# Kernel optimization log

Measured on AMD Instinct MI355X. Metric: run time of the kernel, lower is better.

The kernel has to match this reference:

```python
import jax, jax.numpy as jnp
import numpy as np

N_NODES = 50000
DEGREE = 32
NUM_FEATS = 128
NUM_HIDDEN = 128
NUM_LABELS = 40


def setup_inputs() -> dict:
    key = jax.random.key(0)
    k1, k2, k3, k4, k5, k6 = jax.random.split(key, 6)
    feats = jax.random.normal(k1, (N_NODES, NUM_FEATS), dtype=jnp.float32)
    neigh = jax.random.randint(k2, (N_NODES, DEGREE), 0, N_NODES, dtype=jnp.int32)
    batch = jnp.arange(N_NODES, dtype=jnp.int32)
    s1 = 1.0 / np.sqrt(2 * NUM_FEATS)
    s2 = 1.0 / np.sqrt(2 * NUM_HIDDEN)
    W1 = jax.random.uniform(k3, (2 * NUM_FEATS, NUM_HIDDEN), jnp.float32, -s1, s1)
    b1 = jax.random.uniform(k4, (NUM_HIDDEN,), jnp.float32, -s1, s1)
    W2 = jax.random.uniform(k5, (2 * NUM_HIDDEN, NUM_LABELS), jnp.float32, -s2, s2)
    b2 = jax.random.uniform(k6, (NUM_LABELS,), jnp.float32, -s2, s2)
    return {"feats": feats, "neigh": neigh, "batch": batch,
            "W1": W1, "b1": b1, "W2": W2, "b2": b2}


def reference(feats, neigh, batch, W1, b1, W2, b2):
    # Layer 1 (GraphConvolution with mean aggregator, relu; dropout in eval mode = identity).
    # Compute gc1 embeddings for ALL nodes once: identical math to the per-node
    # Python loop since the mean aggregator is deterministic.
    nbr_mean1 = jnp.take(feats, neigh, axis=0).mean(axis=1)          # [N, F]
    z1 = jnp.concatenate([feats, nbr_mean1], axis=-1)                # [N, 2F]
    h1 = jax.nn.relu(z1 @ W1 + b1)                                   # [N, H]
    # Layer 2 (no activation): concat self embedding with mean of neighbor embeddings.
    nbr_mean2 = jnp.take(h1, neigh[batch], axis=0).mean(axis=1)      # [B, H]
    z2 = jnp.concatenate([h1[batch], nbr_mean2], axis=-1)            # [B, 2H]
    return z2 @ W2 + b2                                              # [B, L]
```

## Files before the change

### kernel.cpp

```cpp
#include <hip/hip_runtime.h>
#include <hip/hip_bf16.h>

typedef __attribute__((ext_vector_type(8))) short short8;
typedef __attribute__((ext_vector_type(4))) float f32x4;

#define NFEAT 128
#define DEG 32
#define FSCALE 24.0f
#define FDEC (1.0f / (24.0f * 32.0f))
#define YSCALE 64.0f
#define YDEC (1.0f / (64.0f * 32.0f))

static __device__ __forceinline__ unsigned short f2bf(float f) {
    unsigned u = __float_as_uint(f);
    u += 0x7fffu + ((u >> 16) & 1u);
    return (unsigned short)(u >> 16);
}
static __device__ __forceinline__ int sxt8(unsigned x) {
    return (int)(signed char)(x & 0xffu);
}

__global__ void prep_feats_kernel(const float* __restrict__ in,
                                  unsigned short* __restrict__ outb,
                                  unsigned* __restrict__ out8, int n4) {
    int i = blockIdx.x * blockDim.x + threadIdx.x;
    if (i >= n4) return;
    float4 f = ((const float4*)in)[i];
    ushort4 ob;
    ob.x = f2bf(f.x); ob.y = f2bf(f.y); ob.z = f2bf(f.z); ob.w = f2bf(f.w);
    ((ushort4*)outb)[i] = ob;
    int a = max(-127, min(127, __float2int_rn(f.x * FSCALE)));
    int b = max(-127, min(127, __float2int_rn(f.y * FSCALE)));
    int c = max(-127, min(127, __float2int_rn(f.z * FSCALE)));
    int d = max(-127, min(127, __float2int_rn(f.w * FSCALE)));
    out8[i] = (unsigned)(a & 0xff) | ((unsigned)(b & 0xff) << 8) |
              ((unsigned)(c & 0xff) << 16) | ((unsigned)(d & 0xff) << 24);
}

__global__ void pack_w1_kernel(const float* __restrict__ W,
                               unsigned short* __restrict__ out) {
    int t = blockIdx.x * blockDim.x + threadIdx.x;
    if (t >= 8 * 8 * 64 * 8) return;
    int j    = t & 7;
    int lane = (t >> 3) & 63;
    int ks   = (t >> 9) & 7;
    int nt   = t >> 12;
    int k    = ks * 32 + (lane >> 4) * 8 + j;
    int col  = nt * 16 + (lane & 15);
    out[t] = f2bf(W[k * 128 + col]);
}

__global__ void pack_w2_kernel(const float* __restrict__ W2,
                               unsigned short* __restrict__ out, int L) {
    int t = blockIdx.x * blockDim.x + threadIdx.x;
    if (t >= 7 * 4 * 64 * 8) return;
    int j    = t & 7;
    int lane = (t >> 3) & 63;
    int ks   = (t >> 9) & 3;
    int nt   = t >> 11;
    int k    = ks * 32 + (lane >> 4) * 8 + j;
    int p    = nt * 16 + (lane & 15);
    float v = 0.f;
    if (p < 48) { if (p < L) v = W2[k * L + p]; }
    else        { int c = p - 48; if (c < L) v = W2[(128 + k) * L + c]; }
    out[t] = f2bf(v);
}

__global__ __launch_bounds__(256, 4) void gcn_layer1_kernel(
    const unsigned short* __restrict__ tableb,
    const unsigned char* __restrict__ table8,
    const int* __restrict__ neigh,
    const unsigned short* __restrict__ Wp,
    const float* __restrict__ bias,
    unsigned short* __restrict__ outp,
    int nRows)
{
    __shared__ unsigned int z1[16 * 128];
    const int tid = threadIdx.x;
    const int w = tid >> 6;
    const int l = tid & 63;
    const int g = l >> 4;
    const int c = l & 15;

    int srow = tid >> 4, sch = tid & 15;
    int sr = min(blockIdx.x * 16 + srow, nRows - 1);
    uint4 selfv = ((const uint4*)(tableb + (size_t)sr * NFEAT))[sch];

    const int r0 = blockIdx.x * 16 + w * 4;
    const int rc0 = min(r0 + 0, nRows - 1);
    const int rc1 = min(r0 + 1, nRows - 1);
    const int rc2 = min(r0 + 2, nRows - 1);
    const int rc3 = min(r0 + 3, nRows - 1);
    const int4* nb0 = (const int4*)(neigh + (size_t)rc0 * DEG);
    const int4* nb1 = (const int4*)(neigh + (size_t)rc1 * DEG);
    const int4* nb2 = (const int4*)(neigh + (size_t)rc2 * DEG);
    const int4* nb3 = (const int4*)(neigh + (size_t)rc3 * DEG);
    int4 ia0 = nb0[2 * g], ib0 = nb0[2 * g + 1];
    int4 ia1 = nb1[2 * g], ib1 = nb1[2 * g + 1];
    int4 ia2 = nb2[2 * g], ib2 = nb2[2 * g + 1];
    int4 ia3 = nb3[2 * g], ib3 = nb3[2 * g + 1];

    const char* tb8 = (const char*)table8;
    const size_t co8 = (size_t)(8 * c);
#define GLD(j) (*(const uint2*)(tb8 + (size_t)(j) * 128 + co8))
#define GATH(A, ia, ib) \
    uint2 A##0 = GLD(ia.x), A##1 = GLD(ia.y), A##2 = GLD(ia.z), A##3 = GLD(ia.w); \
    uint2 A##4 = GLD(ib.x), A##5 = GLD(ib.y), A##6 = GLD(ib.z), A##7 = GLD(ib.w);

    GATH(vA, ia0, ib0)
    GATH(vB, ia1, ib1)

    *(uint4*)((char*)z1 + srow * 512 + ((16 * sch) ^ ((srow & 7) << 4))) = selfv;

    int iacc[8];
#define CONSUME(A, rowi)                                                         \
    {                                                                            \
        _Pragma("unroll") for (int k = 0; k < 8; ++k) iacc[k] = 0;               \
        _Pragma("unroll") for (int q = 0; q < 8; ++q) {                          \
            uint2 v = (q==0)?A##0:(q==1)?A##1:(q==2)?A##2:(q==3)?A##3             \
                    :(q==4)?A##4:(q==5)?A##5:(q==6)?A##6:A##7;                   \
            unsigned x = v.x, y = v.y;                                           \
            iacc[0] += sxt8(x);       iacc[1] += sxt8(x >> 8);                   \
            iacc[2] += sxt8(x >> 16); iacc[3] += sxt8(x >> 24);                  \
            iacc[4] += sxt8(y);       iacc[5] += sxt8(y >> 8);                   \
            iacc[6] += sxt8(y >> 16); iacc[7] += sxt8(y >> 24);                  \
        }                                                                        \
        _Pragma("unroll") for (int k = 0; k < 8; ++k) iacc[k] += __shfl_xor(iacc[k], 16); \
        _Pragma("unroll") for (int k = 0; k < 8; ++k) iacc[k] += __shfl_xor(iacc[k], 32); \
        if (g == 0) {                                                            \
            int row = w * 4 + rowi;                                              \
            uint4 mb;                                                            \
            unsigned* mw = (unsigned*)&mb;                                       \
            _Pragma("unroll") for (int k = 0; k < 4; ++k) {                      \
                unsigned lo = f2bf((float)iacc[2 * k] * FDEC);                   \
                unsigned hi = f2bf((float)iacc[2 * k + 1] * FDEC);               \
                mw[k] = (hi << 16) | lo;                                         \
            }                                                                    \
            int byte = (256 + 16 * c) ^ ((row & 7) << 4);                        \
            *(uint4*)((char*)z1 + row * 512 + byte) = mb;                        \
        }                                                                        \
    }

    CONSUME(vA, 0)
    GATH(vC, ia2, ib2)
    CONSUME(vB, 1)
    GATH(vD, ia3, ib3)
    CONSUME(vC, 2)
    CONSUME(vD, 3)
#undef GLD
#undef GATH
#undef CONSUME
    __syncthreads();

    f32x4 macc0 = (f32x4){0.f,0.f,0.f,0.f}, macc1 = (f32x4){0.f,0.f,0.f,0.f};
    const int arow = l & 15;
    const int aswz = (arow & 7) << 4;
    const char* zbase = (const char*)z1 + arow * 512;

#pragma unroll
    for (int ks = 0; ks < 8; ++ks) {
        int kb = (ks * 64 + ((l >> 4) * 16)) ^ aswz;
        short8 a = *(const short8*)(zbase + kb);
        short8 b0 = *(const short8*)(Wp + ((size_t)((w * 2 + 0) * 8 + ks) * 64 + l) * 8);
        short8 b1 = *(const short8*)(Wp + ((size_t)((w * 2 + 1) * 8 + ks) * 64 + l) * 8);
        macc0 = __builtin_amdgcn_mfma_f32_16x16x32_bf16(a, b0, macc0, 0, 0, 0);
        macc1 = __builtin_amdgcn_mfma_f32_16x16x32_bf16(a, b1, macc1, 0, 0, 0);
    }

#pragma unroll
    for (int tt = 0; tt < 2; ++tt) {
        int col = (w * 2 + tt) * 16 + (l & 15);
        float bv = bias[col];
        f32x4 m = tt ? macc1 : macc0;
#pragma unroll
        for (int r2 = 0; r2 < 4; ++r2) {
            int row = blockIdx.x * 16 + (l >> 4) * 4 + r2;
            if (row < nRows) {
                float v = fmaxf(m[r2] + bv, 0.f);
                outp[(size_t)row * NFEAT + col] = f2bf(v);
            }
        }
    }
}

__global__ __launch_bounds__(256) void gemm2_kernel(
    const unsigned short* __restrict__ h1b,
    const unsigned short* __restrict__ W2p,
    const float* __restrict__ b2,
    float* __restrict__ X2,
    signed char* __restrict__ Y2,
    int nRows, int L)
{
    __shared__ unsigned int lds[64 * 64];
    const int tid = threadIdx.x, w = tid >> 6, l = tid & 63;

#pragma unroll
    for (int it = 0; it < 4; ++it) {
        int byte = tid * 16 + it * 4096;
        int row = byte >> 8, col = byte & 255;
        int r = min(blockIdx.x * 64 + row, nRows - 1);
        uint4 v = *(const uint4*)(h1b + (size_t)r * 128 + (col >> 1));
        *(uint4*)((char*)lds + row * 256 + (col ^ ((row & 7) << 4))) = v;
    }
    __syncthreads();

    f32x4 acc[7];
#pragma unroll
    for (int nt = 0; nt < 7; ++nt) acc[nt] = (f32x4){0.f,0.f,0.f,0.f};
    const int arow = w * 16 + (l & 15);
    const int aswz = (arow & 7) << 4;
    const char* zb = (const char*)lds + arow * 256;

#pragma unroll
    for (int ks = 0; ks < 4; ++ks) {
        short8 a = *(const short8*)(zb + ((ks * 64 + ((l >> 4) * 16)) ^ aswz));
#pragma unroll
        for (int nt = 0; nt < 7; ++nt) {
            short8 b = *(const short8*)(W2p + ((size_t)(nt * 4 + ks) * 64 + l) * 8);
            acc[nt] = __builtin_amdgcn_mfma_f32_16x16x32_bf16(a, b, acc[nt], 0, 0, 0);
        }
    }

#pragma unroll
    for (int nt = 0; nt < 7; ++nt) {
        int col = nt * 16 + (l & 15);
#pragma unroll
        for (int r2 = 0; r2 < 4; ++r2) {
            int row = blockIdx.x * 64 + w * 16 + (l >> 4) * 4 + r2;
            if (row >= nRows) continue;
            float v = acc[nt][r2];
            if (col < 48) {
                if (col < L) X2[(size_t)row * L + col] = v + b2[col];
            } else {
                int q = max(-127, min(127, __float2int_rn(v * YSCALE)));
                Y2[(size_t)row * 64 + (col - 48)] = (signed char)q;
            }
        }
    }
}

__global__ __launch_bounds__(256) void agg2_kernel(
    const float* __restrict__ X2,
    const unsigned char* __restrict__ Y2,
    const int* __restrict__ neigh,
    const int* __restrict__ batch,
    float* __restrict__ out,
    int nRows, int L)
{
    const int tid = threadIdx.x, w = tid >> 6, l = tid & 63;
    const int jg = l >> 3;
    const int c = l & 7;

    const int r0 = blockIdx.x * 16 + w * 4;
    int s[4];
    const int* nb[4];
#pragma unroll
    for (int rr = 0; rr < 4; ++rr) {
        int rc = min(r0 + rr, nRows - 1);
        s[rr] = batch[rc];
        nb[rr] = neigh + (size_t)s[rr] * DEG;
    }
    const char* yb = (const char*)Y2;
    const size_t co = (size_t)(8 * c);
#define YLD(j) (*(const uint2*)(yb + (size_t)(j) * 64 + co))

    uint2 v0[4], v1[4], v2[4], v3[4];
#pragma unroll
    for (int rr = 0; rr < 4; ++rr) {
        v0[rr] = YLD(nb[rr][jg]);
        v1[rr] = YLD(nb[rr][8 + jg]);
        v2[rr] = YLD(nb[rr][16 + jg]);
        v3[rr] = YLD(nb[rr][24 + jg]);
    }
#undef YLD

#pragma unroll
    for (int rr = 0; rr < 4; ++rr) {
        int iacc[8];
#pragma unroll
        for (int k = 0; k < 8; ++k) iacc[k] = 0;
#pragma unroll
        for (int q = 0; q < 4; ++q) {
            uint2 v = (q == 0) ? v0[rr] : (q == 1) ? v1[rr] : (q == 2) ? v2[rr] : v3[rr];
            unsigned x = v.x, y = v.y;
            iacc[0] += sxt8(x);       iacc[1] += sxt8(x >> 8);
            iacc[2] += sxt8(x >> 16); iacc[3] += sxt8(x >> 24);
            iacc[4] += sxt8(y);       iacc[5] += sxt8(y >> 8);
            iacc[6] += sxt8(y >> 16); iacc[7] += sxt8(y >> 24);
        }
#pragma unroll
        for (int k = 0; k < 8; ++k) {
            iacc[k] += __shfl_xor(iacc[k], 8);
            iacc[k] += __shfl_xor(iacc[k], 16);
            iacc[k] += __shfl_xor(iacc[k], 32);
        }
        int r = r0 + rr;
        if (jg == 0 && 8 * c < L && r < nRows) {
#pragma unroll
            for (int hv = 0; hv < 2; ++hv) {
                int colb = 8 * c + 4 * hv;
                if (colb < L) {
                    float4 xv = *(const float4*)(X2 + (size_t)s[rr] * L + colb);
                    float4 o;
                    o.x = xv.x + (float)iacc[4 * hv + 0] * YDEC;
                    o.y = xv.y + (float)iacc[4 * hv + 1] * YDEC;
                    o.z = xv.z + (float)iacc[4 * hv + 2] * YDEC;
                    o.w = xv.w + (float)iacc[4 * hv + 3] * YDEC;
                    *(float4*)(out + (size_t)r * L + colb) = o;
                }
            }
        }
    }
}

extern "C" void kernel_launch(void* const* d_in, const int* in_sizes, int n_in,
                              void* d_out, int out_size, void* d_ws, size_t ws_size,
                              hipStream_t stream) {
    const float* feats = (const float*)d_in[0];
    const int*   neigh = (const int*)d_in[1];
    const int*   batch = (const int*)d_in[2];
    const float* W1    = (const float*)d_in[3];
    const float* b1    = (const float*)d_in[4];
    const float* W2    = (const float*)d_in[5];
    const float* b2    = (const float*)d_in[6];

    const int N = in_sizes[0] / NFEAT;
    const int B = in_sizes[2];
    const int L = in_sizes[6];

    char* ws = (char*)d_ws;
    size_t off = 0;
    unsigned short* featsb = (unsigned short*)(ws + off); off += (size_t)N * NFEAT * 2;
    unsigned short* h1b    = (unsigned short*)(ws + off); off += (size_t)N * NFEAT * 2;
    float*          X2     = (float*)(ws + off);          off += (size_t)N * L * 4;
    signed char*    Y2     = (signed char*)(ws + off);    off += (size_t)N * 64;
    unsigned char*  feats8 = (unsigned char*)(ws + off);  off += (size_t)N * NFEAT;
    unsigned short* W1p    = (unsigned short*)(ws + off); off += 8 * 8 * 64 * 8 * 2;
    unsigned short* W2p    = (unsigned short*)(ws + off); off += 7 * 4 * 64 * 8 * 2;

    int n4 = N * NFEAT / 4;
    prep_feats_kernel<<<(n4 + 255) / 256, 256, 0, stream>>>(
        feats, featsb, (unsigned*)feats8, n4);
    pack_w1_kernel<<<(8 * 8 * 64 * 8 + 255) / 256, 256, 0, stream>>>(W1, W1p);
    pack_w2_kernel<<<(7 * 4 * 64 * 8 + 255) / 256, 256, 0, stream>>>(W2, W2p, L);

    gcn_layer1_kernel<<<(N + 15) / 16, 256, 0, stream>>>(
        featsb, feats8, neigh, W1p, b1, h1b, N);

    gemm2_kernel<<<(N + 63) / 64, 256, 0, stream>>>(
        h1b, W2p, b2, X2, Y2, N, L);

    agg2_kernel<<<(B + 15) / 16, 256, 0, stream>>>(
        X2, (const unsigned char*)Y2, neigh, batch, (float*)d_out, B, L);
}
```

Measured before the change: 149.6 us.

## Fuse layer-1 GEMM with layer-2 projection and merge prep kernels

Layer 1 and the second-layer GEMM now run in one kernel: the relu'd h1 tile is written back into shared memory and immediately multiplied by packed W2, so the bf16 h1 buffer is no longer written to or read from global memory. The three prep/pack kernels are merged into one launch, which saves launch overhead. The int8 neighbor gather now loads 16 bytes per lane from 8 neighbor groups instead of 8 bytes from 4. The cost is extra syncthreads and lower per-block GEMM2 efficiency: tiles are 16 rows instead of 64, and one wave computes a single W2 tile.

```diff
diff --git a/kernel.cpp b/kernel.cpp
--- a/kernel.cpp
+++ b/kernel.cpp
@@ -20,215 +20,209 @@
     return (int)(signed char)(x & 0xffu);
 }
 
-__global__ void prep_feats_kernel(const float* __restrict__ in,
-                                  unsigned short* __restrict__ outb,
-                                  unsigned* __restrict__ out8, int n4) {
-    int i = blockIdx.x * blockDim.x + threadIdx.x;
-    if (i >= n4) return;
-    float4 f = ((const float4*)in)[i];
-    ushort4 ob;
-    ob.x = f2bf(f.x); ob.y = f2bf(f.y); ob.z = f2bf(f.z); ob.w = f2bf(f.w);
-    ((ushort4*)outb)[i] = ob;
-    int a = max(-127, min(127, __float2int_rn(f.x * FSCALE)));
-    int b = max(-127, min(127, __float2int_rn(f.y * FSCALE)));
-    int c = max(-127, min(127, __float2int_rn(f.z * FSCALE)));
-    int d = max(-127, min(127, __float2int_rn(f.w * FSCALE)));
-    out8[i] = (unsigned)(a & 0xff) | ((unsigned)(b & 0xff) << 8) |
-              ((unsigned)(c & 0xff) << 16) | ((unsigned)(d & 0xff) << 24);
-}
-
-__global__ void pack_w1_kernel(const float* __restrict__ W,
-                               unsigned short* __restrict__ out) {
-    int t = blockIdx.x * blockDim.x + threadIdx.x;
-    if (t >= 8 * 8 * 64 * 8) return;
-    int j    = t & 7;
-    int lane = (t >> 3) & 63;
-    int ks   = (t >> 9) & 7;
-    int nt   = t >> 12;
-    int k    = ks * 32 + (lane >> 4) * 8 + j;
-    int col  = nt * 16 + (lane & 15);
-    out[t] = f2bf(W[k * 128 + col]);
-}
-
-__global__ void pack_w2_kernel(const float* __restrict__ W2,
-                               unsigned short* __restrict__ out, int L) {
-    int t = blockIdx.x * blockDim.x + threadIdx.x;
-    if (t >= 7 * 4 * 64 * 8) return;
-    int j    = t & 7;
-    int lane = (t >> 3) & 63;
-    int ks   = (t >> 9) & 3;
-    int nt   = t >> 11;
-    int k    = ks * 32 + (lane >> 4) * 8 + j;
-    int p    = nt * 16 + (lane & 15);
-    float v = 0.f;
-    if (p < 48) { if (p < L) v = W2[k * L + p]; }
-    else        { int c = p - 48; if (c < L) v = W2[(128 + k) * L + c]; }
-    out[t] = f2bf(v);
-}
-
-__global__ __launch_bounds__(256, 4) void gcn_layer1_kernel(
+__global__ void prep_all_kernel(const float* __restrict__ feats,
+                                unsigned short* __restrict__ featsb,
+                                unsigned* __restrict__ feats8,
+                                const float* __restrict__ W1,
+                                unsigned short* __restrict__ W1p,
+                                const float* __restrict__ W2,
+                                unsigned short* __restrict__ W2p,
+                                int n4, int nPrepBlocks, int L) {
+    int b = blockIdx.x;
+    if (b < nPrepBlocks) {
+        int i = b * 256 + threadIdx.x;
+        if (i < n4) {
+            float4 f = ((const float4*)feats)[i];
+            ushort4 ob;
+            ob.x = f2bf(f.x); ob.y = f2bf(f.y); ob.z = f2bf(f.z); ob.w = f2bf(f.w);
+            ((ushort4*)featsb)[i] = ob;
+            int a0 = max(-127, min(127, __float2int_rn(f.x * FSCALE)));
+            int a1 = max(-127, min(127, __float2int_rn(f.y * FSCALE)));
+            int a2 = max(-127, min(127, __float2int_rn(f.z * FSCALE)));
+            int a3 = max(-127, min(127, __float2int_rn(f.w * FSCALE)));
+            feats8[i] = (unsigned)(a0 & 0xff) | ((unsigned)(a1 & 0xff) << 8) |
+                        ((unsigned)(a2 & 0xff) << 16) | ((unsigned)(a3 & 0xff) << 24);
+        }
+    } else if (b < nPrepBlocks + 128) {
+        int t = (b - nPrepBlocks) * 256 + threadIdx.x;
+        int j    = t & 7;
+        int lane = (t >> 3) & 63;
+        int ks   = (t >> 9) & 7;
+        int nt   = t >> 12;
+        int k    = ks * 32 + (lane >> 4) * 8 + j;
+        int col  = nt * 16 + (lane & 15);
+        W1p[t] = f2bf(W1[k * 128 + col]);
+    } else {
+        int t = (b - nPrepBlocks - 128) * 256 + threadIdx.x;
+        if (t < 7 * 4 * 64 * 8) {
+            int j    = t & 7;
+            int lane = (t >> 3) & 63;
+            int ks   = (t >> 9) & 3;
+            int nt   = t >> 11;
+            int k    = ks * 32 + (lane >> 4) * 8 + j;
+            int p    = nt * 16 + (lane & 15);
+            float v = 0.f;
+            if (p < 48) { if (p < L) v = W2[k * L + p]; }
+            else        { int cc = p - 48; if (cc < L) v = W2[(128 + k) * L + cc]; }
+            W2p[t] = f2bf(v);
+        }
+    }
+}
+
+__global__ __launch_bounds__(256, 4) void layer1_fused_kernel(
     const unsigned short* __restrict__ tableb,
     const unsigned char* __restrict__ table8,
     const int* __restrict__ neigh,
-    const unsigned short* __restrict__ Wp,
-    const float* __restrict__ bias,
-    unsigned short* __restrict__ outp,
-    int nRows)
-{
-    __shared__ unsigned int z1[16 * 128];
-    const int tid = threadIdx.x;
-    const int w = tid >> 6;
-    const int l = tid & 63;
-    const int g = l >> 4;
-    const int c = l & 15;
-
-    int srow = tid >> 4, sch = tid & 15;
-    int sr = min(blockIdx.x * 16 + srow, nRows - 1);
-    uint4 selfv = ((const uint4*)(tableb + (size_t)sr * NFEAT))[sch];
-
-    const int r0 = blockIdx.x * 16 + w * 4;
-    const int rc0 = min(r0 + 0, nRows - 1);
-    const int rc1 = min(r0 + 1, nRows - 1);
-    const int rc2 = min(r0 + 2, nRows - 1);
-    const int rc3 = min(r0 + 3, nRows - 1);
-    const int4* nb0 = (const int4*)(neigh + (size_t)rc0 * DEG);
-    const int4* nb1 = (const int4*)(neigh + (size_t)rc1 * DEG);
-    const int4* nb2 = (const int4*)(neigh + (size_t)rc2 * DEG);
-    const int4* nb3 = (const int4*)(neigh + (size_t)rc3 * DEG);
-    int4 ia0 = nb0[2 * g], ib0 = nb0[2 * g + 1];
-    int4 ia1 = nb1[2 * g], ib1 = nb1[2 * g + 1];
-    int4 ia2 = nb2[2 * g], ib2 = nb2[2 * g + 1];
-    int4 ia3 = nb3[2 * g], ib3 = nb3[2 * g + 1];
-
-    const char* tb8 = (const char*)table8;
-    const size_t co8 = (size_t)(8 * c);
-#define GLD(j) (*(const uint2*)(tb8 + (size_t)(j) * 128 + co8))
-#define GATH(A, ia, ib) \
-    uint2 A##0 = GLD(ia.x), A##1 = GLD(ia.y), A##2 = GLD(ia.z), A##3 = GLD(ia.w); \
-    uint2 A##4 = GLD(ib.x), A##5 = GLD(ib.y), A##6 = GLD(ib.z), A##7 = GLD(ib.w);
-
-    GATH(vA, ia0, ib0)
-    GATH(vB, ia1, ib1)
-
-    *(uint4*)((char*)z1 + srow * 512 + ((16 * sch) ^ ((srow & 7) << 4))) = selfv;
-
-    int iacc[8];
-#define CONSUME(A, rowi)                                                         \
-    {                                                                            \
-        _Pragma("unroll") for (int k = 0; k < 8; ++k) iacc[k] = 0;               \
-        _Pragma("unroll") for (int q = 0; q < 8; ++q) {                          \
-            uint2 v = (q==0)?A##0:(q==1)?A##1:(q==2)?A##2:(q==3)?A##3             \
-                    :(q==4)?A##4:(q==5)?A##5:(q==6)?A##6:A##7;                   \
-            unsigned x = v.x, y = v.y;                                           \
-            iacc[0] += sxt8(x);       iacc[1] += sxt8(x >> 8);                   \
-            iacc[2] += sxt8(x >> 16); iacc[3] += sxt8(x >> 24);                  \
-            iacc[4] += sxt8(y);       iacc[5] += sxt8(y >> 8);                   \
-            iacc[6] += sxt8(y >> 16); iacc[7] += sxt8(y >> 24);                  \
-        }                                                                        \
-        _Pragma("unroll") for (int k = 0; k < 8; ++k) iacc[k] += __shfl_xor(iacc[k], 16); \
-        _Pragma("unroll") for (int k = 0; k < 8; ++k) iacc[k] += __shfl_xor(iacc[k], 32); \
-        if (g == 0) {                                                            \
-            int row = w * 4 + rowi;                                              \
-            uint4 mb;                                                            \
-            unsigned* mw = (unsigned*)&mb;                                       \
-            _Pragma("unroll") for (int k = 0; k < 4; ++k) {                      \
-                unsigned lo = f2bf((float)iacc[2 * k] * FDEC);                   \
-                unsigned hi = f2bf((float)iacc[2 * k + 1] * FDEC);               \
-                mw[k] = (hi << 16) | lo;                                         \
-            }                                                                    \
-            int byte = (256 + 16 * c) ^ ((row & 7) << 4);                        \
-            *(uint4*)((char*)z1 + row * 512 + byte) = mb;                        \
-        }                                                                        \
-    }
-
-    CONSUME(vA, 0)
-    GATH(vC, ia2, ib2)
-    CONSUME(vB, 1)
-    GATH(vD, ia3, ib3)
-    CONSUME(vC, 2)
-    CONSUME(vD, 3)
-#undef GLD
-#undef GATH
-#undef CONSUME
-    __syncthreads();
-
-    f32x4 macc0 = (f32x4){0.f,0.f,0.f,0.f}, macc1 = (f32x4){0.f,0.f,0.f,0.f};
-    const int arow = l & 15;
-    const int aswz = (arow & 7) << 4;
-    const char* zbase = (const char*)z1 + arow * 512;
-
-#pragma unroll
-    for (int ks = 0; ks < 8; ++ks) {
-        int kb = (ks * 64 + ((l >> 4) * 16)) ^ aswz;
-        short8 a = *(const short8*)(zbase + kb);
-        short8 b0 = *(const short8*)(Wp + ((size_t)((w * 2 + 0) * 8 + ks) * 64 + l) * 8);
-        short8 b1 = *(const short8*)(Wp + ((size_t)((w * 2 + 1) * 8 + ks) * 64 + l) * 8);
-        macc0 = __builtin_amdgcn_mfma_f32_16x16x32_bf16(a, b0, macc0, 0, 0, 0);
-        macc1 = __builtin_amdgcn_mfma_f32_16x16x32_bf16(a, b1, macc1, 0, 0, 0);
-    }
-
-#pragma unroll
-    for (int tt = 0; tt < 2; ++tt) {
-        int col = (w * 2 + tt) * 16 + (l & 15);
-        float bv = bias[col];
-        f32x4 m = tt ? macc1 : macc0;
-#pragma unroll
-        for (int r2 = 0; r2 < 4; ++r2) {
-            int row = blockIdx.x * 16 + (l >> 4) * 4 + r2;
-            if (row < nRows) {
-                float v = fmaxf(m[r2] + bv, 0.f);
-                outp[(size_t)row * NFEAT + col] = f2bf(v);
-            }
-        }
-    }
-}
-
-__global__ __launch_bounds__(256) void gemm2_kernel(
-    const unsigned short* __restrict__ h1b,
+    const unsigned short* __restrict__ W1p,
+    const float* __restrict__ b1,
     const unsigned short* __restrict__ W2p,
     const float* __restrict__ b2,
     float* __restrict__ X2,
     signed char* __restrict__ Y2,
     int nRows, int L)
 {
-    __shared__ unsigned int lds[64 * 64];
-    const int tid = threadIdx.x, w = tid >> 6, l = tid & 63;
-
-#pragma unroll
-    for (int it = 0; it < 4; ++it) {
-        int byte = tid * 16 + it * 4096;
-        int row = byte >> 8, col = byte & 255;
-        int r = min(blockIdx.x * 64 + row, nRows - 1);
-        uint4 v = *(const uint4*)(h1b + (size_t)r * 128 + (col >> 1));
-        *(uint4*)((char*)lds + row * 256 + (col ^ ((row & 7) << 4))) = v;
-    }
+    __shared__ unsigned int z1[16 * 128];
+    const int tid = threadIdx.x;
+    const int w = tid >> 6;
+    const int l = tid & 63;
+    const int jg = l >> 3;
+    const int c = l & 7;
+
+    int srow = tid >> 4, sch = tid & 15;
+    int sr = min(blockIdx.x * 16 + srow, nRows - 1);
+    uint4 selfv = ((const uint4*)(tableb + (size_t)sr * NFEAT))[sch];
+
+    const int r0 = blockIdx.x * 16 + w * 4;
+    const int* nbp0 = neigh + (size_t)min(r0 + 0, nRows - 1) * DEG;
+    const int* nbp1 = neigh + (size_t)min(r0 + 1, nRows - 1) * DEG;
+    const int* nbp2 = neigh + (size_t)min(r0 + 2, nRows - 1) * DEG;
+    const int* nbp3 = neigh + (size_t)min(r0 + 3, nRows - 1) * DEG;
+    int i00 = nbp0[jg], i01 = nbp0[8 + jg], i02 = nbp0[16 + jg], i03 = nbp0[24 + jg];
+    int i10 = nbp1[jg], i11 = nbp1[8 + jg], i12 = nbp1[16 + jg], i13 = nbp1[24 + jg];
+    int i20 = nbp2[jg], i21 = nbp2[8 + jg], i22 = nbp2[16 + jg], i23 = nbp2[24 + jg];
+    int i30 = nbp3[jg], i31 = nbp3[8 + jg], i32 = nbp3[16 + jg], i33 = nbp3[24 + jg];
+
+    const char* tb8 = (const char*)table8;
+    const size_t co = (size_t)(16 * c);
+#define GLD16(j) (*(const uint4*)(tb8 + (size_t)(j) * 128 + co))
+#define GATH4(A, a, b_, c_, d_) \
+    uint4 A##0 = GLD16(a), A##1 = GLD16(b_), A##2 = GLD16(c_), A##3 = GLD16(d_);
+
+    GATH4(vA, i00, i01, i02, i03)
+    GATH4(vB, i10, i11, i12, i13)
+
+    *(uint4*)((char*)z1 + srow * 512 + ((16 * sch) ^ ((srow & 7) << 4))) = selfv;
+
+    GATH4(vC, i20, i21, i22, i23)
+
+    int iacc[16];
+#define UNPK(v)                                                        \
+    {                                                                  \
+        iacc[0]  += sxt8(v.x);       iacc[1]  += sxt8(v.x >> 8);       \
+        iacc[2]  += sxt8(v.x >> 16); iacc[3]  += sxt8(v.x >> 24);      \
+        iacc[4]  += sxt8(v.y);       iacc[5]  += sxt8(v.y >> 8);       \
+        iacc[6]  += sxt8(v.y >> 16); iacc[7]  += sxt8(v.y >> 24);      \
+        iacc[8]  += sxt8(v.z);       iacc[9]  += sxt8(v.z >> 8);       \
+        iacc[10] += sxt8(v.z >> 16); iacc[11] += sxt8(v.z >> 24);      \
+        iacc[12] += sxt8(v.w);       iacc[13] += sxt8(v.w >> 8);       \
+        iacc[14] += sxt8(v.w >> 16); iacc[15] += sxt8(v.w >> 24);      \
+    }
+#define CONSUME16(A, rowi)                                                        \
+    {                                                                             \
+        _Pragma("unroll") for (int k = 0; k < 16; ++k) iacc[k] = 0;               \
+        UNPK(A##0) UNPK(A##1) UNPK(A##2) UNPK(A##3)                               \
+        _Pragma("unroll") for (int k = 0; k < 16; ++k) iacc[k] += __shfl_xor(iacc[k], 8);  \
+        _Pragma("unroll") for (int k = 0; k < 16; ++k) iacc[k] += __shfl_xor(iacc[k], 16); \
+        _Pragma("unroll") for (int k = 0; k < 16; ++k) iacc[k] += __shfl_xor(iacc[k], 32); \
+        if (jg == 0) {                                                            \
+            int row = w * 4 + rowi;                                               \
+            int swz = (row & 7) << 4;                                             \
+            uint4 m0, m1;                                                         \
+            unsigned* mw0 = (unsigned*)&m0;                                       \
+            unsigned* mw1 = (unsigned*)&m1;                                       \
+            _Pragma("unroll") for (int k = 0; k < 4; ++k) {                       \
+                mw0[k] = ((unsigned)f2bf((float)iacc[2 * k + 1] * FDEC) << 16) |  \
+                         (unsigned)f2bf((float)iacc[2 * k] * FDEC);               \
+                mw1[k] = ((unsigned)f2bf((float)iacc[2 * k + 9] * FDEC) << 16) |  \
+                         (unsigned)f2bf((float)iacc[2 * k + 8] * FDEC);           \
+            }                                                                     \
+            *(uint4*)((char*)z1 + row * 512 + ((256 + 32 * c) ^ swz)) = m0;       \
+            *(uint4*)((char*)z1 + row * 512 + ((256 + 32 * c + 16) ^ swz)) = m1;  \
+        }                                                                         \
+    }
+
+    CONSUME16(vA, 0)
+    GATH4(vD, i30, i31, i32, i33)
+    CONSUME16(vB, 1)
+    CONSUME16(vC, 2)
+    CONSUME16(vD, 3)
+#undef GLD16
+#undef GATH4
+#undef UNPK
+#undef CONSUME16
     __syncthreads();
 
-    f32x4 acc[7];
-#pragma unroll
-    for (int nt = 0; nt < 7; ++nt) acc[nt] = (f32x4){0.f,0.f,0.f,0.f};
-    const int arow = w * 16 + (l & 15);
-    const int aswz = (arow & 7) << 4;
-    const char* zb = (const char*)lds + arow * 256;
-
-#pragma unroll
-    for (int ks = 0; ks < 4; ++ks) {
-        short8 a = *(const short8*)(zb + ((ks * 64 + ((l >> 4) * 16)) ^ aswz));
-#pragma unroll
-        for (int nt = 0; nt < 7; ++nt) {
-            short8 b = *(const short8*)(W2p + ((size_t)(nt * 4 + ks) * 64 + l) * 8);
-            acc[nt] = __builtin_amdgcn_mfma_f32_16x16x32_bf16(a, b, acc[nt], 0, 0, 0);
-        }
-    }
-
-#pragma unroll
-    for (int nt = 0; nt < 7; ++nt) {
+    f32x4 macc0 = (f32x4){0.f,0.f,0.f,0.f}, macc1 = (f32x4){0.f,0.f,0.f,0.f};
+    {
+        const int arow = l & 15;
+        const int aswz = (arow & 7) << 4;
+        const char* zbase = (const char*)z1 + arow * 512;
+#pragma unroll
+        for (int ks = 0; ks < 8; ++ks) {
+            int kb = (ks * 64 + ((l >> 4) * 16)) ^ aswz;
+            short8 a = *(const short8*)(zbase + kb);
+            short8 b0 = *(const short8*)(W1p + ((size_t)((w * 2 + 0) * 8 + ks) * 64 + l) * 8);
+            short8 b1f = *(const short8*)(W1p + ((size_t)((w * 2 + 1) * 8 + ks) * 64 + l) * 8);
+            macc0 = __builtin_amdgcn_mfma_f32_16x16x32_bf16(a, b0, macc0, 0, 0, 0);
+            macc1 = __builtin_amdgcn_mfma_f32_16x16x32_bf16(a, b1f, macc1, 0, 0, 0);
+        }
+    }
+    __syncthreads();
+
+#pragma unroll
+    for (int tt = 0; tt < 2; ++tt) {
+        int col = (w * 2 + tt) * 16 + (l & 15);
+        float bv = b1[col];
+        f32x4 m = tt ? macc1 : macc0;
+#pragma unroll
+        for (int r2 = 0; r2 < 4; ++r2) {
+            int row = (l >> 4) * 4 + r2;
+            float v = fmaxf(m[r2] + bv, 0.f);
+            int byte = row * 256 + ((col * 2) ^ ((row & 7) << 4));
+            *(unsigned short*)((char*)z1 + byte) = f2bf(v);
+        }
+    }
+    __syncthreads();
+
+    f32x4 acc2a = (f32x4){0.f,0.f,0.f,0.f}, acc2b = (f32x4){0.f,0.f,0.f,0.f};
+    {
+        const int arow = l & 15;
+        const int aswz = (arow & 7) << 4;
+        const char* hb = (const char*)z1 + arow * 256;
+        const int ntA = w, ntB = 4 + w;
+#pragma unroll
+        for (int ks2 = 0; ks2 < 4; ++ks2) {
+            short8 a = *(const short8*)(hb + ((ks2 * 64 + ((l >> 4) * 16)) ^ aswz));
+            short8 bA = *(const short8*)(W2p + ((size_t)(ntA * 4 + ks2) * 64 + l) * 8);
+            acc2a = __builtin_amdgcn_mfma_f32_16x16x32_bf16(a, bA, acc2a, 0, 0, 0);
+            if (ntB < 7) {
+                short8 bB = *(const short8*)(W2p + ((size_t)(ntB * 4 + ks2) * 64 + l) * 8);
+                acc2b = __builtin_amdgcn_mfma_f32_16x16x32_bf16(a, bB, acc2b, 0, 0, 0);
+            }
+        }
+    }
+
+#pragma unroll
+    for (int part = 0; part < 2; ++part) {
+        int nt = part ? (4 + w) : w;
+        if (nt >= 7) continue;
+        f32x4 av = part ? acc2b : acc2a;
         int col = nt * 16 + (l & 15);
 #pragma unroll
         for (int r2 = 0; r2 < 4; ++r2) {
-            int row = blockIdx.x * 64 + w * 16 + (l >> 4) * 4 + r2;
+            int row = blockIdx.x * 16 + (l >> 4) * 4 + r2;
             if (row >= nRows) continue;
-            float v = acc[nt][r2];
+            float v = av[r2];
             if (col < 48) {
                 if (col < L) X2[(size_t)row * L + col] = v + b2[col];
             } else {
@@ -263,7 +257,6 @@
     const char* yb = (const char*)Y2;
     const size_t co = (size_t)(8 * c);
 #define YLD(j) (*(const uint2*)(yb + (size_t)(j) * 64 + co))
-
     uint2 v0[4], v1[4], v2[4], v3[4];
 #pragma unroll
     for (int rr = 0; rr < 4; ++rr) {
@@ -331,7 +324,6 @@
     char* ws = (char*)d_ws;
     size_t off = 0;
     unsigned short* featsb = (unsigned short*)(ws + off); off += (size_t)N * NFEAT * 2;
-    unsigned short* h1b    = (unsigned short*)(ws + off); off += (size_t)N * NFEAT * 2;
     float*          X2     = (float*)(ws + off);          off += (size_t)N * L * 4;
     signed char*    Y2     = (signed char*)(ws + off);    off += (size_t)N * 64;
     unsigned char*  feats8 = (unsigned char*)(ws + off);  off += (size_t)N * NFEAT;
@@ -339,16 +331,13 @@
     unsigned short* W2p    = (unsigned short*)(ws + off); off += 7 * 4 * 64 * 8 * 2;
 
     int n4 = N * NFEAT / 4;
-    prep_feats_kernel<<<(n4 + 255) / 256, 256, 0, stream>>>(
-        feats, featsb, (unsigned*)feats8, n4);
-    pack_w1_kernel<<<(8 * 8 * 64 * 8 + 255) / 256, 256, 0, stream>>>(W1, W1p);
-    pack_w2_kernel<<<(7 * 4 * 64 * 8 + 255) / 256, 256, 0, stream>>>(W2, W2p, L);
-
-    gcn_layer1_kernel<<<(N + 15) / 16, 256, 0, stream>>>(
-        featsb, feats8, neigh, W1p, b1, h1b, N);
-
-    gemm2_kernel<<<(N + 63) / 64, 256, 0, stream>>>(
-        h1b, W2p, b2, X2, Y2, N, L);
+    int nPrepBlocks = (n4 + 255) / 256;
+    int totalBlocks = nPrepBlocks + 128 + 56;
+    prep_all_kernel<<<totalBlocks, 256, 0, stream>>>(
+        feats, featsb, (unsigned*)feats8, W1, W1p, W2, W2p, n4, nPrepBlocks, L);
+
+    layer1_fused_kernel<<<(N + 15) / 16, 256, 0, stream>>>(
+        featsb, feats8, neigh, W1p, b1, W2p, b2, X2, Y2, N, L);
 
     agg2_kernel<<<(B + 15) / 16, 256, 0, stream>>>(
         X2, (const unsigned char*)Y2, neigh, batch, (float*)d_out, B, L);
```

New measurement: 148.2 us. No clear change (-0.9%).
